# Kernel optimization log

Measured on AMD Instinct MI355X. Metric: run time of the kernel, lower is better.

The kernel has to match this reference:

```python
import jax, jax.numpy as jnp
import numpy as np

B, T_SRC, T_TGT = 2048, 32, 32
D = 512            # d_model
D_SRC, D_TGT = 100, 80
L = 2              # n_layers


def setup_inputs() -> dict:
    key = jax.random.key(0)
    ks = jax.random.split(key, 16)
    s = 1.0 / float(np.sqrt(D))  # torch LSTM init scale
    u = lambda k, shape: jax.random.uniform(k, shape, jnp.float32, -s, s)
    return {
        "src": jax.random.randint(ks[0], (B, T_SRC), 0, D_SRC, dtype=jnp.int32),
        "tgt": jax.random.randint(ks[1], (B, T_TGT), 0, D_TGT, dtype=jnp.int32),
        "enc_emb": jax.random.normal(ks[2], (D_SRC, D), jnp.float32),
        "dec_emb": jax.random.normal(ks[3], (D_TGT, D), jnp.float32),
        "enc_Wih": u(ks[4], (L, 4 * D, D)),
        "enc_Whh": u(ks[5], (L, 4 * D, D)),
        "enc_bih": u(ks[6], (L, 4 * D)),
        "enc_bhh": u(ks[7], (L, 4 * D)),
        "dec_Wih": u(ks[8], (L, 4 * D, D)),
        "dec_Whh": u(ks[9], (L, 4 * D, D)),
        "dec_bih": u(ks[10], (L, 4 * D)),
        "dec_bhh": u(ks[11], (L, 4 * D)),
        "post_W": u(ks[12], (D_TGT, D)),
        "post_b": u(ks[13], (D_TGT,)),
    }


def lstm_cell(x, h, c, Wih, Whh, bih, bhh):
    # PyTorch gate order: i, f, g, o
    gates = x @ Wih.T + bih + h @ Whh.T + bhh  # [B, 4D]
    i, f, g, o = jnp.split(gates, 4, axis=-1)
    c_new = jax.nn.sigmoid(f) * c + jax.nn.sigmoid(i) * jnp.tanh(g)
    h_new = jax.nn.sigmoid(o) * jnp.tanh(c_new)
    return h_new, c_new


def reference(src, tgt, enc_emb, dec_emb, enc_Wih, enc_Whh, enc_bih, enc_bhh,
              dec_Wih, dec_Whh, dec_bih, dec_bhh, post_W, post_b):
    # Eval-mode forward: dropout = identity, teacher forcing disabled
    # (tf = random() < ratio AND self.training is False at inference).
    n_layers = enc_Wih.shape[0]
    Bb = src.shape[0]
    Dm = enc_emb.shape[1]

    # ---- encoder: multi-layer LSTM over src embeddings ----
    x = enc_emb[src].swapaxes(0, 1)  # [T_src, B, D]
    hs, cs = [], []
    z = jnp.zeros((Bb, Dm), x.dtype)
    for l in range(n_layers):
        def step(carry, xt, l=l):
            h, c = carry
            h, c = lstm_cell(xt, h, c, enc_Wih[l], enc_Whh[l], enc_bih[l], enc_bhh[l])
            return (h, c), h
        (hT, cT), x = jax.lax.scan(step, (z, z), x)
        hs.append(hT)
        cs.append(cT)
    h0 = jnp.stack(hs)  # [L, B, D]
    c0 = jnp.stack(cs)  # [L, B, D]

    prev0 = dec_emb[tgt[:, 0]]  # [B, D]

    def dec_step(carry, _):
        h, c, prev = carry
        x = prev
        new_h, new_c = [], []
        for l in range(n_layers):
            hl, cl = lstm_cell(x, h[l], c[l], dec_Wih[l], dec_Whh[l], dec_bih[l], dec_bhh[l])
            new_h.append(hl)
            new_c.append(cl)
            x = hl
        logits = x @ post_W.T + post_b          # [B, d_tgt]
        pred = jnp.argmax(logits, axis=-1)       # [B]
        prev = dec_emb[pred]                     # [B, D]
        return (jnp.stack(new_h), jnp.stack(new_c), prev), logits

    _, out = jax.lax.scan(dec_step, (h0, c0, prev0), None, length=tgt.shape[1])
    return out.swapaxes(0, 1)  # [B, T_tgt, d_tgt]
```

## Files before the change

### kernel.cpp

```cpp
#include <hip/hip_runtime.h>
#include <hip/hip_bf16.h>

#define B_  2048
#define T_  32
#define D_  512
#define G_  2048
#define VT_ 80
#define BD  (B_ * D_)
#define LWE ((size_t)G_ * D_)

typedef _Float16 half8 __attribute__((ext_vector_type(8)));
typedef _Float16 half4_t __attribute__((ext_vector_type(4)));
typedef float    f32x4 __attribute__((ext_vector_type(4)));

static __device__ __forceinline__ float sigm(float x) {
    return 1.0f / (1.0f + expf(-x));
}

__global__ void zero_ws(int4* __restrict__ p, int n) {
    int i = blockIdx.x * blockDim.x + threadIdx.x;
    if (i < n) p[i] = int4{0, 0, 0, 0};
}
__global__ void init_pred(const int* __restrict__ tgt, int* __restrict__ pred) {
    int i = blockIdx.x * blockDim.x + threadIdx.x;
    if (i < B_) pred[i] = tgt[i * T_];
}

__global__ void split_weights(const float* __restrict__ s0, const float* __restrict__ s1,
                              const float* __restrict__ s2, const float* __restrict__ s3,
                              const float* __restrict__ s4, const float* __restrict__ s5,
                              _Float16* __restrict__ Wbase) {
    int g = blockIdx.x * blockDim.x + threadIdx.x;
    int mat = g >> 17;
    int rem = g & 131071;
    int np  = rem >> 6;
    int kq  = rem & 63;
    const float* src = (mat == 0) ? s0 : (mat == 1) ? s1 : (mat == 2) ? s2
                     : (mat == 3) ? s3 : (mat == 4) ? s4 : s5;
    int n = (np & 3) * D_ + (np >> 2);
    const float* sp = src + (size_t)n * D_ + kq * 8;
    float4 v0 = ((const float4*)sp)[0], v1 = ((const float4*)sp)[1];
    float x[8] = {v0.x, v0.y, v0.z, v0.w, v1.x, v1.y, v1.z, v1.w};
    _Float16 hi[8], lo[8];
    #pragma unroll
    for (int u = 0; u < 8; ++u) {
        hi[u] = (_Float16)x[u];
        lo[u] = (_Float16)(x[u] - (float)hi[u]);
    }
    int tile = (np >> 4) * 16 + (kq >> 2);
    int lane = (np & 15) | ((kq & 3) << 4);
    size_t e = (size_t)tile * 512 + (size_t)lane * 8;
    _Float16* Whi = Wbase + (size_t)mat * (2 * LWE);
    _Float16* Wlo = Whi + LWE;
    *(half8*)(Whi + e) = *(half8*)hi;
    *(half8*)(Wlo + e) = *(half8*)lo;
}

__global__ void perm_bias(const float* __restrict__ ebih, const float* __restrict__ ebhh,
                          const float* __restrict__ dbih, const float* __restrict__ dbhh,
                          float* __restrict__ biasP) {
    int i = blockIdx.x * blockDim.x + threadIdx.x;
    int cfg = i >> 11, np = i & 2047;
    int n = (np & 3) * D_ + (np >> 2);
    const float* bi = ((cfg < 2) ? ebih : dbih) + (cfg & 1) * G_;
    const float* bh = ((cfg < 2) ? ebhh : dbhh) + (cfg & 1) * G_;
    biasP[cfg * G_ + np] = bi[n] + bh[n];
}

__global__ __launch_bounds__(256) void compute_P(
    const float* __restrict__ enc_emb, const float* __restrict__ dec_emb,
    const float* __restrict__ encW0,   const float* __restrict__ decW0,
    float* __restrict__ P) {
    __shared__ float es[10][D_];
    __shared__ float part[4][64][10];
    int by = blockIdx.y;
    bool enc = (by < 10);
    int r0 = enc ? by * 10 : 100 + (by - 10) * 10;
    int s0 = enc ? by * 10 : (by - 10) * 10;
    const float* emb = enc ? enc_emb : dec_emb;
    const float* W   = enc ? encW0 : decW0;
    int tid = threadIdx.x;
    #pragma unroll
    for (int it = 0; it < 5; ++it) {
        int i4 = it * 256 + tid;
        int rr = i4 >> 7, cc = i4 & 127;
        ((float4*)es[rr])[cc] = ((const float4*)(emb + (size_t)(s0 + rr) * D_))[cc];
    }
    __syncthreads();
    int o   = tid & 63;
    int seg = tid >> 6;
    int np = blockIdx.x * 64 + o;
    int n = (np & 3) * D_ + (np >> 2);
    const float* wr = W + (size_t)n * D_ + seg * 128;
    float acc[10];
    #pragma unroll
    for (int rr = 0; rr < 10; ++rr) acc[rr] = 0.f;
    for (int k = 0; k < 128; k += 4) {
        float4 w4 = *(const float4*)(wr + k);
        int kb = seg * 128 + k;
        #pragma unroll
        for (int rr = 0; rr < 10; ++rr)
            acc[rr] += es[rr][kb] * w4.x + es[rr][kb+1] * w4.y
                     + es[rr][kb+2] * w4.z + es[rr][kb+3] * w4.w;
    }
    #pragma unroll
    for (int rr = 0; rr < 10; ++rr) part[seg][o][rr] = acc[rr];
    __syncthreads();
    for (int i = tid; i < 640; i += 256) {
        int o2 = i & 63, rr = i >> 6;
        P[(size_t)(r0 + rr) * G_ + blockIdx.x * 64 + o2] =
            (part[0][o2][rr] + part[1][o2][rr]) + (part[2][o2][rr] + part[3][o2][rr]);
    }
}

static __device__ __forceinline__ void load_chunk(
    const _Float16* __restrict__ Ah, const _Float16* __restrict__ Al,
    const _Float16* __restrict__ Wh, const _Float16* __restrict__ Wl,
    int afr, int wfr, int kc, int lane, half8* A8, half8* B8) {
    size_t lo8 = (size_t)lane * 8;
    #pragma unroll
    for (int i = 0; i < 4; ++i) {
        size_t off = (((size_t)(afr + i) * 16 + kc) << 9) + lo8;
        A8[i]     = *(const half8*)(Ah + off);
        A8[4 + i] = *(const half8*)(Al + off);
    }
    #pragma unroll
    for (int j = 0; j < 4; ++j) {
        size_t off = (((size_t)(wfr + j) * 16 + kc) << 9) + lo8;
        B8[j]     = *(const half8*)(Wh + off);
        B8[4 + j] = *(const half8*)(Wl + off);
    }
}
static __device__ __forceinline__ void mfma_chunk(
    const half8* A8, const half8* B8, f32x4 acc[4][4]) {
    #pragma unroll
    for (int i = 0; i < 4; ++i)
        #pragma unroll
        for (int j = 0; j < 4; ++j) {
            acc[i][j] = __builtin_amdgcn_mfma_f32_16x16x32_f16(A8[i], B8[j], acc[i][j], 0, 0, 0);
            acc[i][j] = __builtin_amdgcn_mfma_f32_16x16x32_f16(A8[i], B8[4 + j], acc[i][j], 0, 0, 0);
            acc[i][j] = __builtin_amdgcn_mfma_f32_16x16x32_f16(A8[4 + i], B8[j], acc[i][j], 0, 0, 0);
        }
}

__global__ __launch_bounds__(512, 2) void lstm_cell_mfma(
    const _Float16* __restrict__ a0h, const _Float16* __restrict__ a0l,
    const _Float16* __restrict__ w0h, const _Float16* __restrict__ w0l,
    int kclo0, int kchi0,
    const _Float16* __restrict__ a1h, const _Float16* __restrict__ a1l,
    const _Float16* __restrict__ w1h, const _Float16* __restrict__ w1l,
    int kclo1, int kchi1,
    const float* __restrict__ biasP,
    const float* __restrict__ P,
    const int* __restrict__ idx, int idx_stride, int emb_rows,
    float* __restrict__ c_io,
    _Float16* __restrict__ hh_out, _Float16* __restrict__ hl_out,
    float* __restrict__ hf_out) {
    __shared__ float gf[128][68];
    const int tid  = threadIdx.x;
    const int w    = tid >> 6;
    const int lane = tid & 63;
    const int g    = w >> 2;
    const int mw   = w & 3;
    const int bx   = blockIdx.x;
    const int m0   = blockIdx.y * 256;

    const _Float16* Ah = g ? a1h : a0h;
    const _Float16* Al = g ? a1l : a0l;
    const _Float16* Wh = g ? w1h : w0h;
    const _Float16* Wl = g ? w1l : w0l;
    const int kclo = g ? kclo1 : kclo0;
    const int kchi = g ? kchi1 : kchi0;

    const int afr = (m0 >> 4) + mw * 4;
    const int wfr = bx * 4;

    f32x4 acc[4][4];
    #pragma unroll
    for (int i = 0; i < 4; ++i)
        #pragma unroll
        for (int j = 0; j < 4; ++j) acc[i][j] = f32x4{0.f, 0.f, 0.f, 0.f};

    half8 A0[8], B0[8], A1[8], B1[8];
    load_chunk(Ah, Al, Wh, Wl, afr, wfr, kclo, lane, A0, B0);
    for (int kc = kclo; kc < kchi; kc += 2) {
        load_chunk(Ah, Al, Wh, Wl, afr, wfr, kc + 1, lane, A1, B1);
        mfma_chunk(A0, B0, acc);
        if (kc + 2 < kchi)
            load_chunk(Ah, Al, Wh, Wl, afr, wfr, kc + 2, lane, A0, B0);
        mfma_chunk(A1, B1, acc);
    }

    const int rbase = (lane >> 4) << 2;
    const int cbase = lane & 15;
    for (int p = 0; p < 2; ++p) {
        if (g == 0 && (mw >> 1) == p) {
            #pragma unroll
            for (int i = 0; i < 4; ++i) {
                int mrow = (mw & 1) * 64 + i * 16 + rbase;
                #pragma unroll
                for (int j = 0; j < 4; ++j) {
                    int nc = j * 16 + cbase;
                    #pragma unroll
                    for (int r = 0; r < 4; ++r)
                        gf[mrow + r][nc] = acc[i][j][r];
                }
            }
        }
        __syncthreads();
        if (g == 1 && (mw >> 1) == p) {
            #pragma unroll
            for (int i = 0; i < 4; ++i) {
                int mrow = (mw & 1) * 64 + i * 16 + rbase;
                #pragma unroll
                for (int j = 0; j < 4; ++j) {
                    int nc = j * 16 + cbase;
                    #pragma unroll
                    for (int r = 0; r < 4; ++r)
                        gf[mrow + r][nc] += acc[i][j][r];
                }
            }
        }
        __syncthreads();
        {
            int mr = tid >> 2, q = tid & 3;
            int mg = m0 + p * 128 + mr;
            const float4* brow = (const float4*)(biasP + (bx << 6));
            const float4* Pr = nullptr;
            if (P) {
                int s = idx[mg * idx_stride];
                s = min(max(s, 0), emb_rows - 1);
                Pr = (const float4*)(P + (size_t)s * G_ + (bx << 6));
            }
            float* crow = c_io + (size_t)mg * D_ + (bx << 4) + (q << 2);
            float4 cv = *(float4*)crow;
            float hv[4];
            _Float16 hh4[4], hl4[4];
            #pragma unroll
            for (int e = 0; e < 4; ++e) {
                int dl = (q << 2) + e;
                float4 g4 = *(float4*)&gf[mr][dl << 2];
                float4 b4 = brow[dl];
                float gi = g4.x + b4.x, gF = g4.y + b4.y;
                float gg = g4.z + b4.z, go = g4.w + b4.w;
                if (Pr) {
                    float4 p4 = Pr[dl];
                    gi += p4.x; gF += p4.y; gg += p4.z; go += p4.w;
                }
                float cc = (&cv.x)[e];
                float cn = sigm(gF) * cc + sigm(gi) * tanhf(gg);
                float hn = sigm(go) * tanhf(cn);
                (&cv.x)[e] = cn; hv[e] = hn;
                _Float16 hH = (_Float16)hn;
                hh4[e] = hH;
                hl4[e] = (_Float16)(hn - (float)hH);
            }
            *(float4*)crow = cv;
            int kk = (bx << 4) + (q << 2);
            size_t hoff = ((size_t)((mg >> 4) * 16 + (kk >> 5)) << 9)
                        + (size_t)((mg & 15) | (((kk >> 3) & 3) << 4)) * 8
                        + ((q & 1) << 2);
            *(half4_t*)(hh_out + hoff) = *(half4_t*)hh4;
            *(half4_t*)(hl_out + hoff) = *(half4_t*)hl4;
            if (hf_out) {
                float4 h4 = {hv[0], hv[1], hv[2], hv[3]};
                *(float4*)(hf_out + (size_t)mg * D_ + kk) = h4;
            }
        }
        __syncthreads();
    }
}

__global__ __launch_bounds__(128) void logits_argmax(
    const float* __restrict__ h1, const float* __restrict__ postW,
    const float* __restrict__ postb, float* __restrict__ out,
    int t, int* __restrict__ pred) {
    __shared__ float hs[D_];
    __shared__ float lg[VT_];
    int b = blockIdx.x;
    int tid = threadIdx.x;
    ((float4*)hs)[tid] = ((const float4*)(h1 + (size_t)b * D_))[tid];
    __syncthreads();
    if (tid < VT_) {
        const float* wr = postW + (size_t)tid * D_;
        float a0 = 0.f, a1 = 0.f, a2 = 0.f, a3 = 0.f;
        for (int d0 = 0; d0 < D_; d0 += 16) {
            float4 w0 = *(const float4*)(wr + d0);
            float4 w1 = *(const float4*)(wr + d0 + 4);
            float4 w2 = *(const float4*)(wr + d0 + 8);
            float4 w3 = *(const float4*)(wr + d0 + 12);
            a0 += hs[d0+0]*w0.x + hs[d0+1]*w0.y + hs[d0+2]*w0.z + hs[d0+3]*w0.w;
            a1 += hs[d0+4]*w1.x + hs[d0+5]*w1.y + hs[d0+6]*w1.z + hs[d0+7]*w1.w;
            a2 += hs[d0+8]*w2.x + hs[d0+9]*w2.y + hs[d0+10]*w2.z + hs[d0+11]*w2.w;
            a3 += hs[d0+12]*w3.x + hs[d0+13]*w3.y + hs[d0+14]*w3.z + hs[d0+15]*w3.w;
        }
        lg[tid] = (a0 + a1) + (a2 + a3) + postb[tid];
    }
    __syncthreads();
    if (tid == 0) {
        float best = lg[0]; int bi = 0;
        for (int v = 1; v < VT_; ++v) { float x = lg[v]; if (x > best) { best = x; bi = v; } }
        pred[b] = bi;
    }
    if (tid < VT_)
        out[(size_t)b * (T_ * VT_) + (size_t)t * VT_ + tid] = lg[tid];
}

extern "C" void kernel_launch(void* const* d_in, const int* in_sizes, int n_in,
                              void* d_out, int out_size, void* d_ws, size_t ws_size,
                              hipStream_t stream) {
    (void)in_sizes; (void)n_in; (void)out_size; (void)ws_size;

    const int*   src     = (const int*)d_in[0];
    const int*   tgt     = (const int*)d_in[1];
    const float* enc_emb = (const float*)d_in[2];
    const float* dec_emb = (const float*)d_in[3];
    const float* enc_Wih = (const float*)d_in[4];
    const float* enc_Whh = (const float*)d_in[5];
    const float* enc_bih = (const float*)d_in[6];
    const float* enc_bhh = (const float*)d_in[7];
    const float* dec_Wih = (const float*)d_in[8];
    const float* dec_Whh = (const float*)d_in[9];
    const float* dec_bih = (const float*)d_in[10];
    const float* dec_bhh = (const float*)d_in[11];
    const float* post_W  = (const float*)d_in[12];
    const float* post_b  = (const float*)d_in[13];

    char* wsb = (char*)d_ws;
    int*   pred  = (int*)wsb;
    float* biasB = (float*)(wsb + 16384);
    float* Ptab  = (float*)(wsb + 16384 + 32768);
    char*  zbase = wsb + 16384 + 32768 + 180 * G_ * 4;
    float* C0 = (float*)zbase;
    float* C1 = C0 + BD;
    _Float16* Hh00 = (_Float16*)(C1 + BD);
    _Float16* Hh10 = Hh00 + BD;
    _Float16* Hl00 = Hh10 + BD;
    _Float16* Hl10 = Hl00 + BD;
    _Float16* Hh01 = Hl10 + BD;
    _Float16* Hh11 = Hh01 + BD;
    _Float16* Hl01 = Hh11 + BD;
    _Float16* Hl11 = Hl01 + BD;
    float*    HF   = (float*)(Hl11 + BD);
    _Float16* Wb   = (_Float16*)(HF + BD);

    _Float16* Hhi[2][2] = { { Hh00, Hh01 }, { Hh10, Hh11 } };
    _Float16* Hlo[2][2] = { { Hl00, Hl01 }, { Hl10, Hl11 } };
    float*    Cp[2]     = { C0, C1 };
    auto WP = [&](int m, int pl) { return Wb + (size_t)m * (2 * LWE) + (size_t)pl * LWE; };

    float* out = (float*)d_out;

    zero_ws<<<4096, 256, 0, stream>>>((int4*)zbase, (16 * 1024 * 1024) / 16);
    init_pred<<<8, 256, 0, stream>>>(tgt, pred);
    split_weights<<<3072, 256, 0, stream>>>(
        enc_Whh, enc_Wih + LWE, enc_Whh + LWE,
        dec_Whh, dec_Wih + LWE, dec_Whh + LWE, Wb);
    perm_bias<<<32, 256, 0, stream>>>(enc_bih, enc_bhh, dec_bih, dec_bhh, biasB);
    {
        dim3 gP(32, 18);
        compute_P<<<gP, 256, 0, stream>>>(enc_emb, dec_emb, enc_Wih, dec_Wih, Ptab);
    }

    dim3 grid(G_ / 64, B_ / 256);
    int c0 = 0, c1 = 0;

    for (int t = 0; t < T_; ++t) {
        lstm_cell_mfma<<<grid, 512, 0, stream>>>(
            Hhi[0][c0], Hlo[0][c0], WP(0, 0), WP(0, 1), 0, 8,
            Hhi[0][c0], Hlo[0][c0], WP(0, 0), WP(0, 1), 8, 16,
            biasB + 0 * G_, Ptab, src + t, T_, 100,
            Cp[0], Hhi[0][c0 ^ 1], Hlo[0][c0 ^ 1], nullptr);
        c0 ^= 1;
        lstm_cell_mfma<<<grid, 512, 0, stream>>>(
            Hhi[0][c0], Hlo[0][c0], WP(1, 0), WP(1, 1), 0, 16,
            Hhi[1][c1], Hlo[1][c1], WP(2, 0), WP(2, 1), 0, 16,
            biasB + 1 * G_, nullptr, nullptr, 0, 0,
            Cp[1], Hhi[1][c1 ^ 1], Hlo[1][c1 ^ 1], nullptr);
        c1 ^= 1;
    }

    for (int t = 0; t < T_; ++t) {
        lstm_cell_mfma<<<grid, 512, 0, stream>>>(
            Hhi[0][c0], Hlo[0][c0], WP(3, 0), WP(3, 1), 0, 8,
            Hhi[0][c0], Hlo[0][c0], WP(3, 0), WP(3, 1), 8, 16,
            biasB + 2 * G_, Ptab + (size_t)100 * G_, pred, 1, VT_,
            Cp[0], Hhi[0][c0 ^ 1], Hlo[0][c0 ^ 1], nullptr);
        c0 ^= 1;
        lstm_cell_mfma<<<grid, 512, 0, stream>>>(
            Hhi[0][c0], Hlo[0][c0], WP(4, 0), WP(4, 1), 0, 16,
            Hhi[1][c1], Hlo[1][c1], WP(5, 0), WP(5, 1), 0, 16,
            biasB + 3 * G_, nullptr, nullptr, 0, 0,
            Cp[1], Hhi[1][c1 ^ 1], Hlo[1][c1 ^ 1], HF);
        c1 ^= 1;
        logits_argmax<<<B_, 128, 0, stream>>>(HF, post_W, post_b, out, t, pred);
    }
}
```

Measured before the change: 4.957 ms.

## Wavefront-pipeline encoder layers in one launch and move logits to split-fp16 MFMA

The encoder now runs layer 1 at step t and layer 0 at step t+1 in a single launch, using a z-dimension of two blocks that each pick their own job descriptor. This halves the number of encoder launches and doubles the parallelism per launch. The decoder logits/argmax step is replaced by an MFMA kernel that reads split hi/lo fp16 copies of h1 and post_W, which are pre-split once, so the fp32 HF buffer and its write are dropped. The logits kernel launches only 32 blocks, which may underuse the GPU, and the hi/lo split could change argmax tie behaviour slightly.

After: 4.255 ms. 14.2% less time.

```diff
diff --git a/kernel.cpp b/kernel.cpp
--- a/kernel.cpp
+++ b/kernel.cpp
@@ -56,6 +56,27 @@
     *(half8*)(Wlo + e) = *(half8*)lo;
 }
 
+__global__ void split_postW(const float* __restrict__ pw,
+                            _Float16* __restrict__ Ph, _Float16* __restrict__ Pl) {
+    int g = blockIdx.x * blockDim.x + threadIdx.x;
+    if (g >= VT_ * 64) return;
+    int v = g >> 6, kq = g & 63;
+    const float* sp = pw + (size_t)v * D_ + kq * 8;
+    float4 v0 = ((const float4*)sp)[0], v1 = ((const float4*)sp)[1];
+    float x[8] = {v0.x, v0.y, v0.z, v0.w, v1.x, v1.y, v1.z, v1.w};
+    _Float16 hi[8], lo[8];
+    #pragma unroll
+    for (int u = 0; u < 8; ++u) {
+        hi[u] = (_Float16)x[u];
+        lo[u] = (_Float16)(x[u] - (float)hi[u]);
+    }
+    int tile = (v >> 4) * 16 + (kq >> 2);
+    int lane = (v & 15) | ((kq & 3) << 4);
+    size_t e = (size_t)tile * 512 + (size_t)lane * 8;
+    *(half8*)(Ph + e) = *(half8*)hi;
+    *(half8*)(Pl + e) = *(half8*)lo;
+}
+
 __global__ void perm_bias(const float* __restrict__ ebih, const float* __restrict__ ebhh,
                           const float* __restrict__ dbih, const float* __restrict__ dbhh,
                           float* __restrict__ biasP) {
@@ -143,19 +164,21 @@
         }
 }
 
-__global__ __launch_bounds__(512, 2) void lstm_cell_mfma(
-    const _Float16* __restrict__ a0h, const _Float16* __restrict__ a0l,
-    const _Float16* __restrict__ w0h, const _Float16* __restrict__ w0l,
-    int kclo0, int kchi0,
-    const _Float16* __restrict__ a1h, const _Float16* __restrict__ a1l,
-    const _Float16* __restrict__ w1h, const _Float16* __restrict__ w1l,
-    int kclo1, int kchi1,
-    const float* __restrict__ biasP,
-    const float* __restrict__ P,
-    const int* __restrict__ idx, int idx_stride, int emb_rows,
-    float* __restrict__ c_io,
-    _Float16* __restrict__ hh_out, _Float16* __restrict__ hl_out,
-    float* __restrict__ hf_out) {
+struct CellJob {
+    const _Float16 *a0h, *a0l, *w0h, *w0l;
+    int kclo0, kchi0;
+    const _Float16 *a1h, *a1l, *w1h, *w1l;
+    int kclo1, kchi1;
+    const float *biasP;
+    const float *P;
+    const int  *idx;
+    int idx_stride, emb_rows;
+    float *c_io;
+    _Float16 *hh_out, *hl_out;
+};
+
+__global__ __launch_bounds__(512, 2) void lstm_cell_mfma(CellJob J0, CellJob J1) {
+    const CellJob J = (blockIdx.z == 0) ? J0 : J1;
     __shared__ float gf[128][68];
     const int tid  = threadIdx.x;
     const int w    = tid >> 6;
@@ -165,12 +188,12 @@
     const int bx   = blockIdx.x;
     const int m0   = blockIdx.y * 256;
 
-    const _Float16* Ah = g ? a1h : a0h;
-    const _Float16* Al = g ? a1l : a0l;
-    const _Float16* Wh = g ? w1h : w0h;
-    const _Float16* Wl = g ? w1l : w0l;
-    const int kclo = g ? kclo1 : kclo0;
-    const int kchi = g ? kchi1 : kchi0;
+    const _Float16* Ah = g ? J.a1h : J.a0h;
+    const _Float16* Al = g ? J.a1l : J.a0l;
+    const _Float16* Wh = g ? J.w1h : J.w0h;
+    const _Float16* Wl = g ? J.w1l : J.w0l;
+    const int kclo = g ? J.kclo1 : J.kclo0;
+    const int kchi = g ? J.kchi1 : J.kchi0;
 
     const int afr = (m0 >> 4) + mw * 4;
     const int wfr = bx * 4;
@@ -225,16 +248,15 @@
         {
             int mr = tid >> 2, q = tid & 3;
             int mg = m0 + p * 128 + mr;
-            const float4* brow = (const float4*)(biasP + (bx << 6));
+            const float4* brow = (const float4*)(J.biasP + (bx << 6));
             const float4* Pr = nullptr;
-            if (P) {
-                int s = idx[mg * idx_stride];
-                s = min(max(s, 0), emb_rows - 1);
-                Pr = (const float4*)(P + (size_t)s * G_ + (bx << 6));
+            if (J.P) {
+                int s = J.idx[mg * J.idx_stride];
+                s = min(max(s, 0), J.emb_rows - 1);
+                Pr = (const float4*)(J.P + (size_t)s * G_ + (bx << 6));
             }
-            float* crow = c_io + (size_t)mg * D_ + (bx << 4) + (q << 2);
+            float* crow = J.c_io + (size_t)mg * D_ + (bx << 4) + (q << 2);
             float4 cv = *(float4*)crow;
-            float hv[4];
             _Float16 hh4[4], hl4[4];
             #pragma unroll
             for (int e = 0; e < 4; ++e) {
@@ -250,7 +272,7 @@
                 float cc = (&cv.x)[e];
                 float cn = sigm(gF) * cc + sigm(gi) * tanhf(gg);
                 float hn = sigm(go) * tanhf(cn);
-                (&cv.x)[e] = cn; hv[e] = hn;
+                (&cv.x)[e] = cn;
                 _Float16 hH = (_Float16)hn;
                 hh4[e] = hH;
                 hl4[e] = (_Float16)(hn - (float)hH);
@@ -260,50 +282,97 @@
             size_t hoff = ((size_t)((mg >> 4) * 16 + (kk >> 5)) << 9)
                         + (size_t)((mg & 15) | (((kk >> 3) & 3) << 4)) * 8
                         + ((q & 1) << 2);
-            *(half4_t*)(hh_out + hoff) = *(half4_t*)hh4;
-            *(half4_t*)(hl_out + hoff) = *(half4_t*)hl4;
-            if (hf_out) {
-                float4 h4 = {hv[0], hv[1], hv[2], hv[3]};
-                *(float4*)(hf_out + (size_t)mg * D_ + kk) = h4;
-            }
+            *(half4_t*)(J.hh_out + hoff) = *(half4_t*)hh4;
+            *(half4_t*)(J.hl_out + hoff) = *(half4_t*)hl4;
         }
         __syncthreads();
     }
 }
 
-__global__ __launch_bounds__(128) void logits_argmax(
-    const float* __restrict__ h1, const float* __restrict__ postW,
+__global__ __launch_bounds__(128) void logits_mfma(
+    const _Float16* __restrict__ Ah, const _Float16* __restrict__ Al,
+    const _Float16* __restrict__ Bh, const _Float16* __restrict__ Bl,
     const float* __restrict__ postb, float* __restrict__ out,
     int t, int* __restrict__ pred) {
-    __shared__ float hs[D_];
-    __shared__ float lg[VT_];
-    int b = blockIdx.x;
-    int tid = threadIdx.x;
-    ((float4*)hs)[tid] = ((const float4*)(h1 + (size_t)b * D_))[tid];
+    __shared__ float gf2[64][85];
+    __shared__ float pb[VT_];
+    const int tid = threadIdx.x;
+    const int w = tid >> 6;
+    const int lane = tid & 63;
+    const int m0 = blockIdx.x * 64;
+    const int afr = blockIdx.x * 4;
+
+    f32x4 acc[4][5];
+    #pragma unroll
+    for (int i = 0; i < 4; ++i)
+        #pragma unroll
+        for (int j = 0; j < 5; ++j) acc[i][j] = f32x4{0.f, 0.f, 0.f, 0.f};
+
+    size_t lo8 = (size_t)lane * 8;
+    for (int kc = w * 8; kc < w * 8 + 8; ++kc) {
+        half8 A8[8], Bh8[5], Bl8[5];
+        #pragma unroll
+        for (int i = 0; i < 4; ++i) {
+            size_t off = (((size_t)(afr + i) * 16 + kc) << 9) + lo8;
+            A8[i]     = *(const half8*)(Ah + off);
+            A8[4 + i] = *(const half8*)(Al + off);
+        }
+        #pragma unroll
+        for (int j = 0; j < 5; ++j) {
+            size_t off = (((size_t)(j * 16 + kc)) << 9) + lo8;
+            Bh8[j] = *(const half8*)(Bh + off);
+            Bl8[j] = *(const half8*)(Bl + off);
+        }
+        #pragma unroll
+        for (int i = 0; i < 4; ++i)
+            #pragma unroll
+            for (int j = 0; j < 5; ++j) {
+                acc[i][j] = __builtin_amdgcn_mfma_f32_16x16x32_f16(A8[i], Bh8[j], acc[i][j], 0, 0, 0);
+                acc[i][j] = __builtin_amdgcn_mfma_f32_16x16x32_f16(A8[i], Bl8[j], acc[i][j], 0, 0, 0);
+                acc[i][j] = __builtin_amdgcn_mfma_f32_16x16x32_f16(A8[4 + i], Bh8[j], acc[i][j], 0, 0, 0);
+            }
+    }
+
+    if (tid < VT_) pb[tid] = postb[tid];
+    const int quad = lane >> 4, c = lane & 15;
+    if (w == 0) {
+        #pragma unroll
+        for (int i = 0; i < 4; ++i)
+            #pragma unroll
+            for (int j = 0; j < 5; ++j)
+                #pragma unroll
+                for (int r = 0; r < 4; ++r)
+                    gf2[i * 16 + quad * 4 + r][j * 16 + c] = acc[i][j][r];
+    }
     __syncthreads();
-    if (tid < VT_) {
-        const float* wr = postW + (size_t)tid * D_;
-        float a0 = 0.f, a1 = 0.f, a2 = 0.f, a3 = 0.f;
-        for (int d0 = 0; d0 < D_; d0 += 16) {
-            float4 w0 = *(const float4*)(wr + d0);
-            float4 w1 = *(const float4*)(wr + d0 + 4);
-            float4 w2 = *(const float4*)(wr + d0 + 8);
-            float4 w3 = *(const float4*)(wr + d0 + 12);
-            a0 += hs[d0+0]*w0.x + hs[d0+1]*w0.y + hs[d0+2]*w0.z + hs[d0+3]*w0.w;
-            a1 += hs[d0+4]*w1.x + hs[d0+5]*w1.y + hs[d0+6]*w1.z + hs[d0+7]*w1.w;
-            a2 += hs[d0+8]*w2.x + hs[d0+9]*w2.y + hs[d0+10]*w2.z + hs[d0+11]*w2.w;
-            a3 += hs[d0+12]*w3.x + hs[d0+13]*w3.y + hs[d0+14]*w3.z + hs[d0+15]*w3.w;
-        }
-        lg[tid] = (a0 + a1) + (a2 + a3) + postb[tid];
+    if (w == 1) {
+        #pragma unroll
+        for (int i = 0; i < 4; ++i)
+            #pragma unroll
+            for (int j = 0; j < 5; ++j)
+                #pragma unroll
+                for (int r = 0; r < 4; ++r)
+                    gf2[i * 16 + quad * 4 + r][j * 16 + c] += acc[i][j][r];
     }
     __syncthreads();
-    if (tid == 0) {
-        float best = lg[0]; int bi = 0;
-        for (int v = 1; v < VT_; ++v) { float x = lg[v]; if (x > best) { best = x; bi = v; } }
-        pred[b] = bi;
-    }
-    if (tid < VT_)
-        out[(size_t)b * (T_ * VT_) + (size_t)t * VT_ + tid] = lg[tid];
+    if (tid < 64) {
+        int r = tid;
+        float best = -3.4e38f; int bi = 0;
+        #pragma unroll
+        for (int v = 0; v < VT_; ++v) {
+            float x = gf2[r][v] + pb[v];
+            if (x > best) { best = x; bi = v; }
+        }
+        pred[m0 + r] = bi;
+        float* orow = out + (size_t)(m0 + r) * (T_ * VT_) + (size_t)t * VT_;
+        #pragma unroll
+        for (int v4 = 0; v4 < VT_ / 4; ++v4) {
+            float4 g4 = *(float4*)&gf2[r][v4 * 4];
+            float4 b4 = *(float4*)&pb[v4 * 4];
+            float4 o4 = {g4.x + b4.x, g4.y + b4.y, g4.z + b4.z, g4.w + b4.w};
+            *(float4*)(orow + v4 * 4) = o4;
+        }
+    }
 }
 
 extern "C" void kernel_launch(void* const* d_in, const int* in_sizes, int n_in,
@@ -341,8 +410,9 @@
     _Float16* Hh11 = Hh01 + BD;
     _Float16* Hl01 = Hh11 + BD;
     _Float16* Hl11 = Hl01 + BD;
-    float*    HF   = (float*)(Hl11 + BD);
-    _Float16* Wb   = (_Float16*)(HF + BD);
+    _Float16* Wb   = Hl11 + BD;
+    _Float16* PwH  = Wb + 6 * 2 * LWE;
+    _Float16* PwL  = PwH + (size_t)VT_ * D_;
 
     _Float16* Hhi[2][2] = { { Hh00, Hh01 }, { Hh10, Hh11 } };
     _Float16* Hlo[2][2] = { { Hl00, Hl01 }, { Hl10, Hl11 } };
@@ -356,43 +426,72 @@
     split_weights<<<3072, 256, 0, stream>>>(
         enc_Whh, enc_Wih + LWE, enc_Whh + LWE,
         dec_Whh, dec_Wih + LWE, dec_Whh + LWE, Wb);
+    split_postW<<<20, 256, 0, stream>>>(post_W, PwH, PwL);
     perm_bias<<<32, 256, 0, stream>>>(enc_bih, enc_bhh, dec_bih, dec_bhh, biasB);
     {
         dim3 gP(32, 18);
         compute_P<<<gP, 256, 0, stream>>>(enc_emb, dec_emb, enc_Wih, dec_Wih, Ptab);
     }
 
-    dim3 grid(G_ / 64, B_ / 256);
+    dim3 grid1(G_ / 64, B_ / 256, 1);
+    dim3 grid2(G_ / 64, B_ / 256, 2);
     int c0 = 0, c1 = 0;
 
+    auto mkL0 = [&](bool enc, const int* ix, int stride, int rows) {
+        int m = enc ? 0 : 3;
+        CellJob j;
+        j.a0h = Hhi[0][c0]; j.a0l = Hlo[0][c0];
+        j.w0h = WP(m, 0);   j.w0l = WP(m, 1);
+        j.kclo0 = 0; j.kchi0 = 8;
+        j.a1h = Hhi[0][c0]; j.a1l = Hlo[0][c0];
+        j.w1h = WP(m, 0);   j.w1l = WP(m, 1);
+        j.kclo1 = 8; j.kchi1 = 16;
+        j.biasP = biasB + (enc ? 0 : 2) * G_;
+        j.P = enc ? Ptab : Ptab + (size_t)100 * G_;
+        j.idx = ix; j.idx_stride = stride; j.emb_rows = rows;
+        j.c_io = Cp[0];
+        j.hh_out = Hhi[0][c0 ^ 1]; j.hl_out = Hlo[0][c0 ^ 1];
+        return j;
+    };
+    auto mkL1 = [&](bool enc) {
+        int mi = enc ? 1 : 4, mh = enc ? 2 : 5;
+        CellJob j;
+        j.a0h = Hhi[0][c0]; j.a0l = Hlo[0][c0];
+        j.w0h = WP(mi, 0);  j.w0l = WP(mi, 1);
+        j.kclo0 = 0; j.kchi0 = 16;
+        j.a1h = Hhi[1][c1]; j.a1l = Hlo[1][c1];
+        j.w1h = WP(mh, 0);  j.w1l = WP(mh, 1);
+        j.kclo1 = 0; j.kchi1 = 16;
+        j.biasP = biasB + (enc ? 1 : 3) * G_;
+        j.P = nullptr; j.idx = nullptr; j.idx_stride = 0; j.emb_rows = 0;
+        j.c_io = Cp[1];
+        j.hh_out = Hhi[1][c1 ^ 1]; j.hl_out = Hlo[1][c1 ^ 1];
+        return j;
+    };
+
+    {
+        CellJob j0 = mkL0(true, src + 0, T_, 100);
+        lstm_cell_mfma<<<grid1, 512, 0, stream>>>(j0, j0);
+        c0 ^= 1;
+        for (int t = 0; t < T_ - 1; ++t) {
+            CellJob jA = mkL1(true);
+            CellJob jB = mkL0(true, src + t + 1, T_, 100);
+            lstm_cell_mfma<<<grid2, 512, 0, stream>>>(jA, jB);
+            c1 ^= 1; c0 ^= 1;
+        }
+        CellJob jZ = mkL1(true);
+        lstm_cell_mfma<<<grid1, 512, 0, stream>>>(jZ, jZ);
+        c1 ^= 1;
+    }
+
     for (int t = 0; t < T_; ++t) {
-        lstm_cell_mfma<<<grid, 512, 0, stream>>>(
-            Hhi[0][c0], Hlo[0][c0], WP(0, 0), WP(0, 1), 0, 8,
-            Hhi[0][c0], Hlo[0][c0], WP(0, 0), WP(0, 1), 8, 16,
-            biasB + 0 * G_, Ptab, src + t, T_, 100,
-            Cp[0], Hhi[0][c0 ^ 1], Hlo[0][c0 ^ 1], nullptr);
+        CellJob j0 = mkL0(false, pred, 1, VT_);
+        lstm_cell_mfma<<<grid1, 512, 0, stream>>>(j0, j0);
         c0 ^= 1;
-        lstm_cell_mfma<<<grid, 512, 0, stream>>>(
-            Hhi[0][c0], Hlo[0][c0], WP(1, 0), WP(1, 1), 0, 16,
-            Hhi[1][c1], Hlo[1][c1], WP(2, 0), WP(2, 1), 0, 16,
-            biasB + 1 * G_, nullptr, nullptr, 0, 0,
-            Cp[1], Hhi[1][c1 ^ 1], Hlo[1][c1 ^ 1], nullptr);
+        CellJob j1 = mkL1(false);
+        lstm_cell_mfma<<<grid1, 512, 0, stream>>>(j1, j1);
         c1 ^= 1;
-    }
-
-    for (int t = 0; t < T_; ++t) {
-        lstm_cell_mfma<<<grid, 512, 0, stream>>>(
-            Hhi[0][c0], Hlo[0][c0], WP(3, 0), WP(3, 1), 0, 8,
-            Hhi[0][c0], Hlo[0][c0], WP(3, 0), WP(3, 1), 8, 16,
-            biasB + 2 * G_, Ptab + (size_t)100 * G_, pred, 1, VT_,
-            Cp[0], Hhi[0][c0 ^ 1], Hlo[0][c0 ^ 1], nullptr);
-        c0 ^= 1;
-        lstm_cell_mfma<<<grid, 512, 0, stream>>>(
-            Hhi[0][c0], Hlo[0][c0], WP(4, 0), WP(4, 1), 0, 16,
-            Hhi[1][c1], Hlo[1][c1], WP(5, 0), WP(5, 1), 0, 16,
-            biasB + 3 * G_, nullptr, nullptr, 0, 0,
-            Cp[1], Hhi[1][c1 ^ 1], Hlo[1][c1 ^ 1], HF);
-        c1 ^= 1;
-        logits_argmax<<<B_, 128, 0, stream>>>(HF, post_W, post_b, out, t, pred);
-    }
-}
+        logits_mfma<<<32, 128, 0, stream>>>(
+            Hhi[1][c1], Hlo[1][c1], PwH, PwL, post_b, out, t, pred);
+    }
+}
```
